# Kernel tuning notes

Hardware: AMD Instinct MI355X
Metric: run time of the kernel (lower is better)

The kernel has to match this reference:

```python
import jax, jax.numpy as jnp
import numpy as np

# Llama-3.2-1B-style int4-quantized decoder (4 layers, reduced vocab)
L, D, H, HD, KVH, DFF, V, B, S = 4, 2048, 32, 64, 8, 8192, 32000, 4, 1024
ROPE_THETA = 500000.0


def setup_inputs() -> dict:
    key = jax.random.key(0)
    ks = jax.random.split(key, 18)
    def qw(k, shape):  # int4 weights stored in int32 carrier, range [-8, 8)
        return jax.random.randint(k, shape, -8, 8, dtype=jnp.int32)
    def sc(k, shape):  # per-output-channel dequant scales
        return jax.random.uniform(k, shape, jnp.float32, 0.005, 0.02)
    DKV = KVH * HD
    return {
        "token_ids": jax.random.randint(ks[0], (B, S), 0, V, dtype=jnp.int32),
        "embed": jax.random.normal(ks[1], (V, D), jnp.float32) * 0.02,
        "gamma_attn": jnp.ones((L, D), jnp.float32),
        "gamma_mlp": jnp.ones((L, D), jnp.float32),
        "gamma_final": jnp.ones((D,), jnp.float32),
        "wq": qw(ks[2], (L, D, D)),   "sq": sc(ks[3], (L, D)),
        "wk": qw(ks[4], (L, DKV, D)), "sk": sc(ks[5], (L, DKV)),
        "wv": qw(ks[6], (L, DKV, D)), "sv": sc(ks[7], (L, DKV)),
        "wo": qw(ks[8], (L, D, D)),   "so": sc(ks[9], (L, D)),
        "wg": qw(ks[10], (L, DFF, D)), "sg": sc(ks[11], (L, DFF)),
        "wu": qw(ks[12], (L, DFF, D)), "su": sc(ks[13], (L, DFF)),
        "wd": qw(ks[14], (L, D, DFF)), "sd": sc(ks[15], (L, D)),
    }


def _rmsnorm(x, g, eps=1e-5):
    return x * jax.lax.rsqrt(jnp.mean(x * x, axis=-1, keepdims=True) + eps) * g


def _rope(x):  # x: [B, S, n_heads, HD], split-half rotation (Llama convention)
    half = HD // 2
    inv_freq = ROPE_THETA ** (-jnp.arange(half, dtype=jnp.float32) * 2.0 / HD)
    ang = jnp.arange(x.shape[1], dtype=jnp.float32)[:, None] * inv_freq  # [S, half]
    cos = jnp.cos(ang)[None, :, None, :]
    sin = jnp.sin(ang)[None, :, None, :]
    x1, x2 = jnp.split(x, 2, axis=-1)
    return jnp.concatenate([x1 * cos - x2 * sin, x1 * sin + x2 * cos], axis=-1)


def _qlin(x, w_int, scale):
    # int4 dequant (per-out-channel symmetric) + matmul: y = x @ (w_int*scale)^T
    w = w_int.astype(jnp.float32) * scale[:, None]
    return jnp.einsum('bsd,od->bso', x, w)


def _forward(token_ids, embed, gamma_attn, gamma_mlp, gamma_final,
             wq, sq, wk, sk, wv, sv, wo, so, wg, sg, wu, su, wd, sd):
    x = embed[token_ids]                                    # [B, S, D]
    causal = jnp.tril(jnp.ones((S, S), dtype=bool))
    for l in range(L):
        # --- attention block ---
        h = _rmsnorm(x, gamma_attn[l])
        q = _qlin(h, wq[l], sq[l]).reshape(B, S, H, HD)
        k = _qlin(h, wk[l], sk[l]).reshape(B, S, KVH, HD)
        v = _qlin(h, wv[l], sv[l]).reshape(B, S, KVH, HD)
        q, k = _rope(q), _rope(k)
        k = jnp.repeat(k, H // KVH, axis=2)                 # GQA expand
        v = jnp.repeat(v, H // KVH, axis=2)
        scores = jnp.einsum('bqhd,bkhd->bhqk', q, k) / np.float32(np.sqrt(HD))
        scores = jnp.where(causal, scores, jnp.float32(-1e9))
        p = jax.nn.softmax(scores, axis=-1)
        attn = jnp.einsum('bhqk,bkhd->bqhd', p, v).reshape(B, S, D)
        x = x + _qlin(attn, wo[l], so[l])
        # --- SwiGLU MLP block ---
        h = _rmsnorm(x, gamma_mlp[l])
        g = jax.nn.silu(_qlin(h, wg[l], sg[l]))
        u = _qlin(h, wu[l], su[l])
        x = x + _qlin(g * u, wd[l], sd[l])
    x = _rmsnorm(x, gamma_final)
    # tied-embedding LM head; next-token logits at last position (decode step)
    return x[:, -1, :] @ embed.T                             # [B, V]


def reference(token_ids, embed, gamma_attn, gamma_mlp, gamma_final,
              wq, sq, wk, sk, wv, sv, wo, so, wg, sg, wu, su, wd, sd):
    return _forward(token_ids, embed, gamma_attn, gamma_mlp, gamma_final,
                    wq, sq, wk, sk, wv, sv, wo, so, wg, sg, wu, su, wd, sd)
```

## Files before the change

kernel.cpp:

```cpp
#include <hip/hip_runtime.h>
#include <hip/hip_bf16.h>

#define D_MODEL 2048
#define NH 32
#define HDIM 64
#define KVHEADS 8
#define DKV 512
#define DFF 8192
#define SEQ 1024
#define BATCH 4
#define NTOK 4096
#define VOCAB 32000
#define NLAYER 4

typedef __attribute__((ext_vector_type(8))) _Float16 f16x8;
typedef __attribute__((ext_vector_type(4))) _Float16 f16x4;
typedef __attribute__((ext_vector_type(4))) float f32x4;
typedef __attribute__((ext_vector_type(4))) int i32x4;

static __device__ __forceinline__ void gload16(const void* g, void* l){
    __builtin_amdgcn_global_load_lds(
        (const __attribute__((address_space(1))) unsigned int*)g,
        (__attribute__((address_space(3))) unsigned int*)l, 16, 0, 0);
}

#define MFMA(d, x, y) d = __builtin_amdgcn_mfma_f32_16x16x32_f16(x, y, d, 0, 0, 0)
#define BAR()    __builtin_amdgcn_s_barrier()
#define LGK0()   do{ asm volatile("s_waitcnt lgkmcnt(0)" ::: "memory"); \
                     __builtin_amdgcn_sched_barrier(0); }while(0)
#define PRIO(x)  __builtin_amdgcn_s_setprio(x)

__global__ __launch_bounds__(256)
void gather_kernel(const int* __restrict__ tok, const float* __restrict__ embed,
                   float* __restrict__ X)
{
    int row = blockIdx.x;
    int id = tok[row];
    const float4* s = (const float4*)(embed + (size_t)id * D_MODEL);
    float4* d = (float4*)(X + (size_t)row * D_MODEL);
    d[threadIdx.x]       = s[threadIdx.x];
    d[threadIdx.x + 256] = s[threadIdx.x + 256];
}

__global__ __launch_bounds__(256)
void rope_table_kernel(float2* __restrict__ rt)
{
    int idx = blockIdx.x * 256 + threadIdx.x;
    int pos = idx >> 5, d = idx & 31;
    float inv = powf(500000.0f, -(float)d * (1.0f / 32.0f));
    float ang = (float)pos * inv;
    float s, c;
    sincosf(ang, &s, &c);
    rt[idx] = make_float2(c, s);
}

__global__ __launch_bounds__(256)
void wconv_all_kernel(const int* __restrict__ wq, const int* __restrict__ wk,
                      const int* __restrict__ wv, const int* __restrict__ wo,
                      const int* __restrict__ wg, const int* __restrict__ wu,
                      const int* __restrict__ wd, _Float16* __restrict__ O)
{
    int i = blockIdx.x * 256 + threadIdx.x;
    const int* s; int loc;
    if      (i <  1048576){ s = wq; loc = i; }
    else if (i <  1310720){ s = wk; loc = i - 1048576; }
    else if (i <  1572864){ s = wv; loc = i - 1310720; }
    else if (i <  2621440){ s = wo; loc = i - 1572864; }
    else if (i <  6815744){ s = wg; loc = i - 2621440; }
    else if (i < 11010048){ s = wu; loc = i - 6815744; }
    else                  { s = wd; loc = i - 11010048; }
    i32x4 w = __builtin_nontemporal_load(&((const i32x4*)s)[loc]);
    f16x4 o;
    o.x = (_Float16)(float)w.x; o.y = (_Float16)(float)w.y;
    o.z = (_Float16)(float)w.z; o.w = (_Float16)(float)w.w;
    __builtin_nontemporal_store(o, &((f16x4*)O)[i]);
}

__global__ __launch_bounds__(256)
void rmsnorm_kernel(const float* __restrict__ X, const float* __restrict__ gamma,
                    _Float16* __restrict__ O)
{
    int row = blockIdx.x;
    const float* x = X + (size_t)row * D_MODEL;
    _Float16* o = O + (size_t)row * D_MODEL;
    int t = threadIdx.x;
    float4 v[2];
    float ss = 0.f;
#pragma unroll
    for (int i = 0; i < 2; i++){
        v[i] = *(const float4*)&x[(t + i*256)*4];
        ss += v[i].x*v[i].x + v[i].y*v[i].y + v[i].z*v[i].z + v[i].w*v[i].w;
    }
    for (int off = 32; off; off >>= 1) ss += __shfl_xor(ss, off, 64);
    __shared__ float red[4];
    __shared__ float invs;
    int lane = t & 63, wid = t >> 6;
    if (lane == 0) red[wid] = ss;
    __syncthreads();
    if (t == 0){
        float s = red[0] + red[1] + red[2] + red[3];
        invs = 1.0f / sqrtf(s / (float)D_MODEL + 1e-5f);
    }
    __syncthreads();
    float inv = invs;
#pragma unroll
    for (int i = 0; i < 2; i++){
        float4 g = *(const float4*)&gamma[(t + i*256)*4];
        f16x4 r;
        r.x = (_Float16)(v[i].x * inv * g.x); r.y = (_Float16)(v[i].y * inv * g.y);
        r.z = (_Float16)(v[i].z * inv * g.z); r.w = (_Float16)(v[i].w * inv * g.w);
        *(f16x4*)&o[(t + i*256)*4] = r;
    }
}

__global__ __launch_bounds__(256)
void final_norm_kernel(const float* __restrict__ X, const float* __restrict__ gamma,
                       float* __restrict__ XF)
{
    int b = blockIdx.x;
    const float* x = X + ((size_t)b * SEQ + SEQ - 1) * D_MODEL;
    float* o = XF + (size_t)b * D_MODEL;
    int t = threadIdx.x;
    float4 v[2];
    float ss = 0.f;
#pragma unroll
    for (int i = 0; i < 2; i++){
        v[i] = *(const float4*)&x[(t + i*256)*4];
        ss += v[i].x*v[i].x + v[i].y*v[i].y + v[i].z*v[i].z + v[i].w*v[i].w;
    }
    for (int off = 32; off; off >>= 1) ss += __shfl_xor(ss, off, 64);
    __shared__ float red[4];
    __shared__ float invs;
    int lane = t & 63, wid = t >> 6;
    if (lane == 0) red[wid] = ss;
    __syncthreads();
    if (t == 0){
        float s = red[0] + red[1] + red[2] + red[3];
        invs = 1.0f / sqrtf(s / (float)D_MODEL + 1e-5f);
    }
    __syncthreads();
    float inv = invs;
#pragma unroll
    for (int i = 0; i < 2; i++){
        float4 g = *(const float4*)&gamma[(t + i*256)*4];
        float4 r;
        r.x = v[i].x * inv * g.x; r.y = v[i].y * inv * g.y;
        r.z = v[i].z * inv * g.z; r.w = v[i].w * inv * g.w;
        *(float4*)&o[(t + i*256)*4] = r;
    }
}

__global__ __launch_bounds__(512, 2)
void gemm_mlp(const _Float16* __restrict__ A, const _Float16* __restrict__ WU,
              const _Float16* __restrict__ WG,
              const float* __restrict__ su, const float* __restrict__ sg,
              _Float16* __restrict__ U, int MT, int NT, int K)
{
    __shared__ __align__(16) _Float16 AS[2][256 * 64];
    __shared__ __align__(16) _Float16 US[2][128 * 64];
    __shared__ __align__(16) _Float16 GS[3][128 * 64];

    int nwg = MT * NT;
    int flat = blockIdx.x;
    int q = nwg >> 3, r = nwg & 7;
    int xcd = flat & 7, lid = flat >> 3;
    int swz = (xcd < r ? xcd * (q + 1) : r * (q + 1) + (xcd - r) * q) + lid;
    int bm = swz % MT, bn = swz / MT;
    int m0 = bm * 256, n0 = bn * 128;

    const int t = threadIdx.x;
    const int lane = t & 63, wid = t >> 6;
    const int ln15 = lane & 15, lq = lane >> 4;
    const int wm = wid >> 1, wn = wid & 1;
    const int sw = ln15 & 7;
    const int sl0 = (lq ^ sw) * 8, sl1 = ((4 + lq) ^ sw) * 8;

    const _Float16* srcA[4]; const _Float16* srcU[2]; const _Float16* srcG[2];
#pragma unroll
    for (int rr = 0; rr < 4; rr++){
        int ch = rr * 512 + t;
        int row = ch >> 3, s = (ch & 7) ^ (row & 7);
        srcA[rr] = A + (size_t)(m0 + row) * K + s * 8;
    }
#pragma unroll
    for (int rr = 0; rr < 2; rr++){
        int ch = rr * 512 + t;
        int row = ch >> 3, s = (ch & 7) ^ (row & 7);
        srcU[rr] = WU + (size_t)(n0 + row) * K + s * 8;
        srcG[rr] = WG + (size_t)(n0 + row) * K + s * 8;
    }
#define STG_A4(tile) do{ int _b = (tile) & 1; \
    gload16(srcA[0] + (size_t)(tile)*64, &AS[_b][(wid*64)*8]); \
    gload16(srcA[1] + (size_t)(tile)*64, &AS[_b][(512 + wid*64)*8]); \
    gload16(srcA[2] + (size_t)(tile)*64, &AS[_b][(1024 + wid*64)*8]); \
    gload16(srcA[3] + (size_t)(tile)*64, &AS[_b][(1536 + wid*64)*8]); }while(0)
#define STG_U2(tile) do{ int _b = (tile) & 1; \
    gload16(srcU[0] + (size_t)(tile)*64, &US[_b][(wid*64)*8]); \
    gload16(srcU[1] + (size_t)(tile)*64, &US[_b][(512 + wid*64)*8]); }while(0)
#define STG_G3(tile) do{ int _b = (tile) % 3; \
    gload16(srcG[0] + (size_t)(tile)*64, &GS[_b][(wid*64)*8]); \
    gload16(srcG[1] + (size_t)(tile)*64, &GS[_b][(512 + wid*64)*8]); }while(0)

    f32x4 accU[4][4], accG[4][4];
#pragma unroll
    for (int i = 0; i < 4; i++)
#pragma unroll
        for (int j = 0; j < 4; j++){
            accU[i][j] = (f32x4){0.f, 0.f, 0.f, 0.f};
            accG[i][j] = (f32x4){0.f, 0.f, 0.f, 0.f};
        }

    const int KT = K >> 6;

    STG_A4(0); STG_U2(0); STG_G3(0); STG_G3(1);
    asm volatile("s_waitcnt vmcnt(2)" ::: "memory");
    BAR();

    for (int kt = 0; kt < KT; ++kt){
        int cur = kt & 1, gcur = kt % 3;
        const _Float16* Ac = AS[cur];
        const _Float16* Uc = US[cur];
        const _Float16* Gc = GS[gcur];
        bool s1 = (kt + 1 < KT), s2 = (kt + 2 < KT);

        f16x8 afk0[4], afk1[4], buk0[4], buk1[4];
#pragma unroll
        for (int mf = 0; mf < 4; mf++)
            afk0[mf] = *(const f16x8*)&Ac[(wm * 64 + mf * 16 + ln15) * 64 + sl0];
#pragma unroll
        for (int nf = 0; nf < 4; nf++)
            buk0[nf] = *(const f16x8*)&Uc[(wn * 64 + nf * 16 + ln15) * 64 + sl0];
        if (s1) STG_A4(kt + 1);
        BAR(); LGK0(); PRIO(1);
#pragma unroll
        for (int mf = 0; mf < 4; mf++)
#pragma unroll
            for (int nf = 0; nf < 4; nf++)
                MFMA(accU[mf][nf], afk0[mf], buk0[nf]);
        PRIO(0); BAR();

#pragma unroll
        for (int mf = 0; mf < 4; mf++)
            afk1[mf] = *(const f16x8*)&Ac[(wm * 64 + mf * 16 + ln15) * 64 + sl1];
#pragma unroll
        for (int nf = 0; nf < 4; nf++)
            buk1[nf] = *(const f16x8*)&Uc[(wn * 64 + nf * 16 + ln15) * 64 + sl1];
        if (s1) STG_U2(kt + 1);
        BAR(); LGK0(); PRIO(1);
#pragma unroll
        for (int mf = 0; mf < 4; mf++)
#pragma unroll
            for (int nf = 0; nf < 4; nf++)
                MFMA(accU[mf][nf], afk1[mf], buk1[nf]);
        PRIO(0); BAR();

        f16x8 bgk0[4], bgk1[4];
#pragma unroll
        for (int nf = 0; nf < 4; nf++){
            bgk0[nf] = *(const f16x8*)&Gc[(wn * 64 + nf * 16 + ln15) * 64 + sl0];
            bgk1[nf] = *(const f16x8*)&Gc[(wn * 64 + nf * 16 + ln15) * 64 + sl1];
        }
        if (s2) STG_G3(kt + 2);
        BAR(); LGK0(); PRIO(1);
#pragma unroll
        for (int mf = 0; mf < 4; mf++)
#pragma unroll
            for (int nf = 0; nf < 4; nf++)
                MFMA(accG[mf][nf], afk0[mf], bgk0[nf]);
        PRIO(0); BAR();

        PRIO(1);
#pragma unroll
        for (int mf = 0; mf < 4; mf++)
#pragma unroll
            for (int nf = 0; nf < 4; nf++)
                MFMA(accG[mf][nf], afk1[mf], bgk1[nf]);
        PRIO(0);
        if (s1){
            if (s2) asm volatile("s_waitcnt vmcnt(2)" ::: "memory");
            else    asm volatile("s_waitcnt vmcnt(0)" ::: "memory");
            BAR();
            __builtin_amdgcn_sched_barrier(0);
        }
    }
#undef STG_A4
#undef STG_U2
#undef STG_G3

#pragma unroll
    for (int mf = 0; mf < 4; mf++){
        int rowb = m0 + wm * 64 + mf * 16 + lq * 4;
#pragma unroll
        for (int nf = 0; nf < 4; nf++){
            int colg = n0 + wn * 64 + nf * 16 + ln15;
            float scu = su[colg], scg = sg[colg];
#pragma unroll
            for (int rr2 = 0; rr2 < 4; rr2++){
                float uv = accU[mf][nf][rr2] * scu;
                float gv = accG[mf][nf][rr2] * scg;
                float sig = 1.0f / (1.0f + expf(-gv));
                U[(size_t)(rowb + rr2) * DFF + colg] = (_Float16)(gv * sig * uv);
            }
        }
    }
}

template<int EPI>
__global__ __launch_bounds__(512, 2)
void gemm_small(const _Float16* __restrict__ A, const _Float16* __restrict__ W,
                const float* __restrict__ sc0, const float* __restrict__ sc1,
                const float* __restrict__ sc2,
                void* __restrict__ C0, void* __restrict__ C1, void* __restrict__ C2,
                const float2* __restrict__ rt,
                int MT, int NT, int N, int K)
{
    __shared__ __align__(16) _Float16 AS[3][128 * 64];
    __shared__ __align__(16) _Float16 BS[3][256 * 64];

    int nwg = MT * NT;
    int flat = blockIdx.x;
    int q = nwg >> 3, r = nwg & 7;
    int xcd = flat & 7, lid = flat >> 3;
    int swz = (xcd < r ? xcd * (q + 1) : r * (q + 1) + (xcd - r) * q) + lid;
    int bm = swz % MT, bn = swz / MT;
    int m0 = bm * 128, n0 = bn * 256;

    const int t = threadIdx.x;
    const int lane = t & 63, wid = t >> 6;
    const int ln15 = lane & 15, lq = lane >> 4;
    const int wm = wid >> 2, wn = wid & 3;
    const int sw = ln15 & 7;
    const int sl0 = (lq ^ sw) * 8, sl1 = ((4 + lq) ^ sw) * 8;

    const _Float16* srcA[2]; const _Float16* srcB[4];
#pragma unroll
    for (int rr = 0; rr < 2; rr++){
        int ch = rr * 512 + t;
        int row = ch >> 3, s = (ch & 7) ^ (row & 7);
        srcA[rr] = A + (size_t)(m0 + row) * K + s * 8;
    }
#pragma unroll
    for (int rr = 0; rr < 4; rr++){
        int ch = rr * 512 + t;
        int row = ch >> 3, s = (ch & 7) ^ (row & 7);
        srcB[rr] = W + (size_t)(n0 + row) * K + s * 8;
    }
#define STG_A3(tile) do{ int _b = (tile) % 3; \
    gload16(srcA[0] + (size_t)(tile)*64, &AS[_b][(wid*64)*8]); \
    gload16(srcA[1] + (size_t)(tile)*64, &AS[_b][(512 + wid*64)*8]); }while(0)
#define STG_B3(tile) do{ int _b = (tile) % 3; \
    gload16(srcB[0] + (size_t)(tile)*64, &BS[_b][(wid*64)*8]); \
    gload16(srcB[1] + (size_t)(tile)*64, &BS[_b][(512 + wid*64)*8]); \
    gload16(srcB[2] + (size_t)(tile)*64, &BS[_b][(1024 + wid*64)*8]); \
    gload16(srcB[3] + (size_t)(tile)*64, &BS[_b][(1536 + wid*64)*8]); }while(0)

    f32x4 acc[4][4];
#pragma unroll
    for (int i = 0; i < 4; i++)
#pragma unroll
        for (int j = 0; j < 4; j++) acc[i][j] = (f32x4){0.f, 0.f, 0.f, 0.f};

    const int KT = K >> 6;

    STG_A3(0); STG_B3(0); STG_A3(1); STG_B3(1);
    asm volatile("s_waitcnt vmcnt(6)" ::: "memory");
    BAR();

    for (int kt = 0; kt < KT; ++kt){
        int cur = kt % 3;
        const _Float16* Ac = AS[cur];
        const _Float16* Bc = BS[cur];
        bool s1 = (kt + 1 < KT), s2 = (kt + 2 < KT);

        f16x8 af0[4], af1[4], bk0[4], bk1[4];
#pragma unroll
        for (int mf = 0; mf < 4; mf++)
            af0[mf] = *(const f16x8*)&Ac[(wm * 64 + mf * 16 + ln15) * 64 + sl0];
#pragma unroll
        for (int nf = 0; nf < 4; nf++)
            bk0[nf] = *(const f16x8*)&Bc[(wn * 64 + nf * 16 + ln15) * 64 + sl0];
        if (s2) STG_B3(kt + 2);
        BAR(); LGK0(); PRIO(1);
#pragma unroll
        for (int mf = 0; mf < 4; mf++)
#pragma unroll
            for (int nf = 0; nf < 4; nf++)
                MFMA(acc[mf][nf], af0[mf], bk0[nf]);
        PRIO(0); BAR();

#pragma unroll
        for (int mf = 0; mf < 4; mf++)
            af1[mf] = *(const f16x8*)&Ac[(wm * 64 + mf * 16 + ln15) * 64 + sl1];
#pragma unroll
        for (int nf = 0; nf < 4; nf++)
            bk1[nf] = *(const f16x8*)&Bc[(wn * 64 + nf * 16 + ln15) * 64 + sl1];
        if (s2) STG_A3(kt + 2);
        BAR(); LGK0(); PRIO(1);
#pragma unroll
        for (int mf = 0; mf < 4; mf++)
#pragma unroll
            for (int nf = 0; nf < 4; nf++)
                MFMA(acc[mf][nf], af1[mf], bk1[nf]);
        PRIO(0);
        if (s1){
            if (s2) asm volatile("s_waitcnt vmcnt(6)" ::: "memory");
            else    asm volatile("s_waitcnt vmcnt(0)" ::: "memory");
            BAR();
            __builtin_amdgcn_sched_barrier(0);
        }
    }
#undef STG_A3
#undef STG_B3

    if (EPI == 3){
        const float* sp; _Float16* dp; int nloc, nstr;
        if (n0 < 2048)      { sp = sc0; dp = (_Float16*)C0; nloc = n0;        nstr = 2048; }
        else if (n0 < 2560) { sp = sc1; dp = (_Float16*)C1; nloc = n0 - 2048; nstr = 512; }
        else                { sp = sc2; dp = (_Float16*)C2; nloc = n0 - 2560; nstr = 512; }
        bool dorope = (n0 < 2560);
        if (dorope){
#pragma unroll
            for (int mf = 0; mf < 4; mf++){
                int rowb = m0 + wm * 64 + mf * 16 + lq * 4;
#pragma unroll
                for (int nf = 0; nf < 2; nf++){
                    int colg = wn * 64 + nf * 16 + ln15;
                    int d = nf * 16 + ln15;
                    float s1v = sp[nloc + colg], s2v = sp[nloc + colg + 32];
#pragma unroll
                    for (int rr2 = 0; rr2 < 4; rr2++){
                        int row = rowb + rr2;
                        int pos = row & (SEQ - 1);
                        float2 cs = rt[pos * 32 + d];
                        float x1 = acc[mf][nf][rr2] * s1v;
                        float x2 = acc[mf][nf + 2][rr2] * s2v;
                        dp[(size_t)row * nstr + nloc + colg]      = (_Float16)(x1 * cs.x - x2 * cs.y);
                        dp[(size_t)row * nstr + nloc + colg + 32] = (_Float16)(x1 * cs.y + x2 * cs.x);
                    }
                }
            }
        } else {
#pragma unroll
            for (int mf = 0; mf < 4; mf++){
                int rowb = m0 + wm * 64 + mf * 16 + lq * 4;
#pragma unroll
                for (int nf = 0; nf < 4; nf++){
                    int colg = wn * 64 + nf * 16 + ln15;
                    float sc = sp[nloc + colg];
#pragma unroll
                    for (int rr2 = 0; rr2 < 4; rr2++)
                        dp[(size_t)(rowb + rr2) * nstr + nloc + colg] =
                            (_Float16)(acc[mf][nf][rr2] * sc);
                }
            }
        }
    } else {
#pragma unroll
        for (int mf = 0; mf < 4; mf++){
            int rowb = m0 + wm * 64 + mf * 16 + lq * 4;
#pragma unroll
            for (int nf = 0; nf < 4; nf++){
                int colg = n0 + wn * 64 + nf * 16 + ln15;
                float sc = sc0[colg];
#pragma unroll
                for (int rr2 = 0; rr2 < 4; rr2++){
                    size_t idx = (size_t)(rowb + rr2) * N + colg;
                    float val = acc[mf][nf][rr2] * sc;
                    if (EPI == 0){
                        ((_Float16*)C0)[idx] = (_Float16)val;
                    } else {
                        ((float*)C0)[idx] += val;
                    }
                }
            }
        }
    }
}

__global__ __launch_bounds__(256)
void attn_kernel(const _Float16* __restrict__ Qb, const _Float16* __restrict__ Kb,
                 const _Float16* __restrict__ Vb, _Float16* __restrict__ Ob)
{
    int bid = blockIdx.x;
    int qt = bid >> 7, h = bid & 31, b = (bid >> 5) & 3;
    int kvh = h >> 2;
    int q0 = qt * 128;
    int t = threadIdx.x, lane = t & 63, wid = t >> 6;
    int ln15 = lane & 15, lq = lane >> 4;

    __shared__ __align__(16) _Float16 Ksm[64 * 72];
    __shared__ __align__(16) _Float16 Vt[64 * 72];
    __shared__ __align__(16) _Float16 Pl[128 * 72];

    f16x8 qf[2][2];
    int qrow_g = b * SEQ + q0 + wid * 32;
#pragma unroll
    for (int mf = 0; mf < 2; mf++)
#pragma unroll
        for (int dc = 0; dc < 2; dc++)
            qf[mf][dc] = *(const f16x8*)(Qb + (size_t)(qrow_g + mf * 16 + ln15) * D_MODEL
                                         + h * HDIM + dc * 32 + lq * 8);

    f32x4 outv[2][4];
#pragma unroll
    for (int i = 0; i < 2; i++)
#pragma unroll
        for (int j = 0; j < 4; j++) outv[i][j] = (f32x4){0.f, 0.f, 0.f, 0.f};
    float mrun[2][4], lrun[2][4];
#pragma unroll
    for (int i = 0; i < 2; i++)
#pragma unroll
        for (int r = 0; r < 4; r++){ mrun[i][r] = -1e30f; lrun[i][r] = 0.f; }

    int ntile = (q0 + 128) >> 6;
    int ld_row = (t + 0) >> 3, ld_c8 = t & 7;
    int ld_row1 = (t + 256) >> 3;

    f16x8 k8[2], v8[2];
    {
        size_t base0 = (size_t)(b * SEQ + ld_row) * DKV + kvh * HDIM + ld_c8 * 8;
        size_t base1 = (size_t)(b * SEQ + ld_row1) * DKV + kvh * HDIM + ld_c8 * 8;
        k8[0] = *(const f16x8*)&Kb[base0];  v8[0] = *(const f16x8*)&Vb[base0];
        k8[1] = *(const f16x8*)&Kb[base1];  v8[1] = *(const f16x8*)&Vb[base1];
    }

    for (int kt = 0; kt < ntile; kt++){
        __syncthreads();
#pragma unroll
        for (int i = 0; i < 2; i++){
            int row = (i == 0) ? ld_row : ld_row1;
            *(f16x8*)&Ksm[row * 72 + ld_c8 * 8] = k8[i];
#pragma unroll
            for (int j = 0; j < 8; j++)
                Vt[(ld_c8 * 8 + j) * 72 + row] = v8[i][j];
        }
        __syncthreads();

        if (kt + 1 < ntile){
            size_t base0 = (size_t)(b * SEQ + (kt + 1) * 64 + ld_row) * DKV + kvh * HDIM + ld_c8 * 8;
            size_t base1 = (size_t)(b * SEQ + (kt + 1) * 64 + ld_row1) * DKV + kvh * HDIM + ld_c8 * 8;
            k8[0] = *(const f16x8*)&Kb[base0];  v8[0] = *(const f16x8*)&Vb[base0];
            k8[1] = *(const f16x8*)&Kb[base1];  v8[1] = *(const f16x8*)&Vb[base1];
        }

#pragma unroll
        for (int mf = 0; mf < 2; mf++){
            f32x4 sa[4];
#pragma unroll
            for (int kvf = 0; kvf < 4; kvf++) sa[kvf] = (f32x4){0.f, 0.f, 0.f, 0.f};
#pragma unroll
            for (int kvf = 0; kvf < 4; kvf++)
#pragma unroll
                for (int dc = 0; dc < 2; dc++){
                    f16x8 kb = *(const f16x8*)&Ksm[(kvf * 16 + ln15) * 72 + dc * 32 + lq * 8];
                    sa[kvf] = __builtin_amdgcn_mfma_f32_16x16x32_f16(qf[mf][dc], kb, sa[kvf], 0, 0, 0);
                }
            int qbase = q0 + wid * 32 + mf * 16 + lq * 4;
            float rowmax[4] = {-1e30f, -1e30f, -1e30f, -1e30f};
#pragma unroll
            for (int kvf = 0; kvf < 4; kvf++){
                int kva = kt * 64 + kvf * 16 + ln15;
#pragma unroll
                for (int r = 0; r < 4; r++){
                    float sv = sa[kvf][r] * 0.125f;
                    if (kva > qbase + r) sv = -1e9f;
                    sa[kvf][r] = sv;
                    rowmax[r] = fmaxf(rowmax[r], sv);
                }
            }
#pragma unroll
            for (int r = 0; r < 4; r++){
                rowmax[r] = fmaxf(rowmax[r], __shfl_xor(rowmax[r], 1, 64));
                rowmax[r] = fmaxf(rowmax[r], __shfl_xor(rowmax[r], 2, 64));
                rowmax[r] = fmaxf(rowmax[r], __shfl_xor(rowmax[r], 4, 64));
                rowmax[r] = fmaxf(rowmax[r], __shfl_xor(rowmax[r], 8, 64));
            }
            float scl[4], rsum[4];
#pragma unroll
            for (int r = 0; r < 4; r++){
                float mo = mrun[mf][r];
                float mn = fmaxf(mo, rowmax[r]);
                scl[r] = expf(mo - mn);
                mrun[mf][r] = mn;
                rsum[r] = 0.f;
            }
#pragma unroll
            for (int kvf = 0; kvf < 4; kvf++)
#pragma unroll
                for (int r = 0; r < 4; r++){
                    float p = expf(sa[kvf][r] - mrun[mf][r]);
                    sa[kvf][r] = p;
                    rsum[r] += p;
                }
#pragma unroll
            for (int r = 0; r < 4; r++){
                rsum[r] += __shfl_xor(rsum[r], 1, 64);
                rsum[r] += __shfl_xor(rsum[r], 2, 64);
                rsum[r] += __shfl_xor(rsum[r], 4, 64);
                rsum[r] += __shfl_xor(rsum[r], 8, 64);
                lrun[mf][r] = lrun[mf][r] * scl[r] + rsum[r];
            }
#pragma unroll
            for (int dfr = 0; dfr < 4; dfr++)
#pragma unroll
                for (int r = 0; r < 4; r++) outv[mf][dfr][r] *= scl[r];
#pragma unroll
            for (int kvf = 0; kvf < 4; kvf++)
#pragma unroll
                for (int r = 0; r < 4; r++)
                    Pl[(wid * 32 + mf * 16 + lq * 4 + r) * 72 + kvf * 16 + ln15] = (_Float16)sa[kvf][r];
        }
        __syncthreads();

#pragma unroll
        for (int mf = 0; mf < 2; mf++)
#pragma unroll
            for (int kc = 0; kc < 2; kc++){
                f16x8 pa = *(const f16x8*)&Pl[(wid * 32 + mf * 16 + ln15) * 72 + kc * 32 + lq * 8];
#pragma unroll
                for (int dfr = 0; dfr < 4; dfr++){
                    f16x8 vb = *(const f16x8*)&Vt[(dfr * 16 + ln15) * 72 + kc * 32 + lq * 8];
                    outv[mf][dfr] = __builtin_amdgcn_mfma_f32_16x16x32_f16(pa, vb, outv[mf][dfr], 0, 0, 0);
                }
            }
    }

#pragma unroll
    for (int mf = 0; mf < 2; mf++)
#pragma unroll
        for (int dfr = 0; dfr < 4; dfr++)
#pragma unroll
            for (int r = 0; r < 4; r++){
                float val = outv[mf][dfr][r] / lrun[mf][r];
                size_t row = (size_t)(b * SEQ + q0 + wid * 32 + mf * 16 + lq * 4 + r);
                Ob[row * D_MODEL + h * HDIM + dfr * 16 + ln15] = (_Float16)val;
            }
}

__global__ __launch_bounds__(256)
void lmhead_kernel(const float* __restrict__ XF, const float* __restrict__ embed,
                   float* __restrict__ out)
{
    __shared__ float xl[4 * D_MODEL];
    int t = threadIdx.x;
#pragma unroll
    for (int i = 0; i < 8; i++){
        int f = t + i * 256;
        ((float4*)xl)[f] = ((const float4*)XF)[f];
    }
    __syncthreads();
    int lane = t & 63, wid = t >> 6;
    for (int rr = 0; rr < 16; rr++){
        int vrow = blockIdx.x * 64 + wid * 16 + rr;
        const float4* er = (const float4*)(embed + (size_t)vrow * D_MODEL);
        float acc[4] = {0.f, 0.f, 0.f, 0.f};
        for (int j = 0; j < 8; j++){
            float4 e = er[lane + 64 * j];
#pragma unroll
            for (int b = 0; b < 4; b++){
                float4 xv = ((float4*)xl)[b * 512 + lane + 64 * j];
                acc[b] += e.x * xv.x + e.y * xv.y + e.z * xv.z + e.w * xv.w;
            }
        }
#pragma unroll
        for (int b = 0; b < 4; b++)
            for (int off = 32; off; off >>= 1) acc[b] += __shfl_xor(acc[b], off, 64);
        if (lane == 0){
#pragma unroll
            for (int b = 0; b < 4; b++)
                out[(size_t)b * VOCAB + vrow] = acc[b];
        }
    }
}

extern "C" void kernel_launch(void* const* d_in, const int* in_sizes, int n_in,
                              void* d_out, int out_size, void* d_ws, size_t ws_size,
                              hipStream_t stream)
{
    const int*   tok   = (const int*)d_in[0];
    const float* embed = (const float*)d_in[1];
    const float* g_attn = (const float*)d_in[2];
    const float* g_mlp  = (const float*)d_in[3];
    const float* g_fin  = (const float*)d_in[4];
    const int*   wq = (const int*)d_in[5];  const float* sq = (const float*)d_in[6];
    const int*   wk = (const int*)d_in[7];  const float* sk = (const float*)d_in[8];
    const int*   wv = (const int*)d_in[9];  const float* sv = (const float*)d_in[10];
    const int*   wo = (const int*)d_in[11]; const float* so = (const float*)d_in[12];
    const int*   wg = (const int*)d_in[13]; const float* sg = (const float*)d_in[14];
    const int*   wu = (const int*)d_in[15]; const float* su = (const float*)d_in[16];
    const int*   wd = (const int*)d_in[17]; const float* sd = (const float*)d_in[18];
    float* out = (float*)d_out;

    char* p = (char*)d_ws;
    _Float16* Wf = (_Float16*)p;  p += (size_t)60817408 * 2;
    float*    X  = (float*)p;     p += (size_t)NTOK * D_MODEL * 4;
    _Float16* Hb = (_Float16*)p;  p += (size_t)NTOK * D_MODEL * 2;
    _Float16* Qb = (_Float16*)p;  p += (size_t)NTOK * D_MODEL * 2;
    _Float16* Kb = (_Float16*)p;  p += (size_t)NTOK * DKV * 2;
    _Float16* Vb = (_Float16*)p;  p += (size_t)NTOK * DKV * 2;
    _Float16* Ab = (_Float16*)p;  p += (size_t)NTOK * D_MODEL * 2;
    _Float16* Ub = (_Float16*)p;  p += (size_t)NTOK * DFF * 2;
    float*    XF = (float*)p;     p += (size_t)BATCH * D_MODEL * 4;
    float2*   RT = (float2*)p;    p += (size_t)SEQ * 32 * 8;

    _Float16* wqf = Wf;
    _Float16* wkf = wqf + (size_t)D_MODEL * D_MODEL;
    _Float16* wvf = wkf + (size_t)DKV * D_MODEL;
    _Float16* wof = wvf + (size_t)DKV * D_MODEL;
    _Float16* wgf = wof + (size_t)D_MODEL * D_MODEL;
    _Float16* wuf = wgf + (size_t)DFF * D_MODEL;
    _Float16* wdf = wuf + (size_t)DFF * D_MODEL;

    gather_kernel<<<NTOK, 256, 0, stream>>>(tok, embed, X);
    rope_table_kernel<<<SEQ * 32 / 256, 256, 0, stream>>>(RT);

    for (int l = 0; l < NLAYER; l++){
        wconv_all_kernel<<<15204352 / 256, 256, 0, stream>>>(
            wq + (size_t)l * D_MODEL * D_MODEL,
            wk + (size_t)l * DKV * D_MODEL,
            wv + (size_t)l * DKV * D_MODEL,
            wo + (size_t)l * D_MODEL * D_MODEL,
            wg + (size_t)l * DFF * D_MODEL,
            wu + (size_t)l * DFF * D_MODEL,
            wd + (size_t)l * D_MODEL * DFF,
            Wf);

        rmsnorm_kernel<<<NTOK, 256, 0, stream>>>(X, g_attn + (size_t)l * D_MODEL, Hb);
        gemm_small<3><<<32 * 12, 512, 0, stream>>>(Hb, wqf,
            sq + (size_t)l * D_MODEL, sk + (size_t)l * DKV, sv + (size_t)l * DKV,
            Qb, Kb, Vb, RT, 32, 12, 3072, D_MODEL);
        attn_kernel<<<1024, 256, 0, stream>>>(Qb, Kb, Vb, Ab);
        gemm_small<1><<<32 * 8, 512, 0, stream>>>(Ab, wof,
            so + (size_t)l * D_MODEL, nullptr, nullptr,
            X, nullptr, nullptr, nullptr, 32, 8, D_MODEL, D_MODEL);

        rmsnorm_kernel<<<NTOK, 256, 0, stream>>>(X, g_mlp + (size_t)l * D_MODEL, Hb);
        gemm_mlp<<<16 * 64, 512, 0, stream>>>(Hb, wuf, wgf,
            su + (size_t)l * DFF, sg + (size_t)l * DFF, Ub, 16, 64, D_MODEL);
        gemm_small<1><<<32 * 8, 512, 0, stream>>>(Ub, wdf,
            sd + (size_t)l * D_MODEL, nullptr, nullptr,
            X, nullptr, nullptr, nullptr, 32, 8, D_MODEL, DFF);
    }

    final_norm_kernel<<<BATCH, 256, 0, stream>>>(X, g_fin, XF);
    lmhead_kernel<<<VOCAB / 64, 256, 0, stream>>>(XF, embed, out);
}
```

Before: 3.211 ms.

## Add split-K 256x256 down-projection GEMM with atomic accumulation into residual

Replaces the gemm_small launch for the MLP down-projection with a new gemm_wd kernel. It reuses the gemm_mlp pipeline structure with a 256x256 output tile, treating the two 128-column halves as the U and G operands. K is split in two across workgroups, which restores the block count to 256 despite the larger tile. Partial results are scaled and added into the residual X with float atomicAdd, trading higher arithmetic intensity for atomic traffic and a non-deterministic summation order.

```diff
diff --git a/kernel.cpp b/kernel.cpp
--- a/kernel.cpp
+++ b/kernel.cpp
@@ -150,6 +150,7 @@
     }
 }
 
+
 __global__ __launch_bounds__(512, 2)
 void gemm_mlp(const _Float16* __restrict__ A, const _Float16* __restrict__ WU,
               const _Float16* __restrict__ WG,
@@ -300,6 +301,164 @@
                 float gv = accG[mf][nf][rr2] * scg;
                 float sig = 1.0f / (1.0f + expf(-gv));
                 U[(size_t)(rowb + rr2) * DFF + colg] = (_Float16)(gv * sig * uv);
+            }
+        }
+    }
+}
+
+__global__ __launch_bounds__(512, 2)
+void gemm_wd(const _Float16* __restrict__ Afull, const _Float16* __restrict__ Wfull,
+             const float* __restrict__ sc, float* __restrict__ C,
+             int MT, int NT, int N, int Kfull)
+{
+    __shared__ __align__(16) _Float16 AS[2][256 * 64];
+    __shared__ __align__(16) _Float16 US[2][128 * 64];
+    __shared__ __align__(16) _Float16 GS[3][128 * 64];
+
+    int flat = blockIdx.x;
+    int kz = flat & 1;
+    int rest = flat >> 1;
+    int nwg = MT * NT;
+    int q = nwg >> 3, r = nwg & 7;
+    int xcd = rest & 7, lid = rest >> 3;
+    int swz = (xcd < r ? xcd * (q + 1) : r * (q + 1) + (xcd - r) * q) + lid;
+    int bm = swz % MT, bn = swz / MT;
+    int m0 = bm * 256, n0 = bn * 256;
+    const int K = Kfull >> 1;
+    const _Float16* A = Afull + (size_t)kz * K;
+    const _Float16* W = Wfull + (size_t)kz * K;
+
+    const int t = threadIdx.x;
+    const int lane = t & 63, wid = t >> 6;
+    const int ln15 = lane & 15, lq = lane >> 4;
+    const int wm = wid >> 1, wn = wid & 1;
+    const int sw = ln15 & 7;
+    const int sl0 = (lq ^ sw) * 8, sl1 = ((4 + lq) ^ sw) * 8;
+
+    const _Float16* srcA[4]; const _Float16* srcU[2]; const _Float16* srcG[2];
+#pragma unroll
+    for (int rr = 0; rr < 4; rr++){
+        int ch = rr * 512 + t;
+        int row = ch >> 3, s = (ch & 7) ^ (row & 7);
+        srcA[rr] = A + (size_t)(m0 + row) * Kfull + s * 8;
+    }
+#pragma unroll
+    for (int rr = 0; rr < 2; rr++){
+        int ch = rr * 512 + t;
+        int row = ch >> 3, s = (ch & 7) ^ (row & 7);
+        srcU[rr] = W + (size_t)(n0 + row) * Kfull + s * 8;
+        srcG[rr] = W + (size_t)(n0 + 128 + row) * Kfull + s * 8;
+    }
+#define STG_A4(tile) do{ int _b = (tile) & 1; \
+    gload16(srcA[0] + (size_t)(tile)*64, &AS[_b][(wid*64)*8]); \
+    gload16(srcA[1] + (size_t)(tile)*64, &AS[_b][(512 + wid*64)*8]); \
+    gload16(srcA[2] + (size_t)(tile)*64, &AS[_b][(1024 + wid*64)*8]); \
+    gload16(srcA[3] + (size_t)(tile)*64, &AS[_b][(1536 + wid*64)*8]); }while(0)
+#define STG_U2(tile) do{ int _b = (tile) & 1; \
+    gload16(srcU[0] + (size_t)(tile)*64, &US[_b][(wid*64)*8]); \
+    gload16(srcU[1] + (size_t)(tile)*64, &US[_b][(512 + wid*64)*8]); }while(0)
+#define STG_G3(tile) do{ int _b = (tile) % 3; \
+    gload16(srcG[0] + (size_t)(tile)*64, &GS[_b][(wid*64)*8]); \
+    gload16(srcG[1] + (size_t)(tile)*64, &GS[_b][(512 + wid*64)*8]); }while(0)
+
+    f32x4 accU[4][4], accG[4][4];
+#pragma unroll
+    for (int i = 0; i < 4; i++)
+#pragma unroll
+        for (int j = 0; j < 4; j++){
+            accU[i][j] = (f32x4){0.f, 0.f, 0.f, 0.f};
+            accG[i][j] = (f32x4){0.f, 0.f, 0.f, 0.f};
+        }
+
+    const int KT = K >> 6;
+
+    STG_A4(0); STG_U2(0); STG_G3(0); STG_G3(1);
+    asm volatile("s_waitcnt vmcnt(2)" ::: "memory");
+    BAR();
+
+    for (int kt = 0; kt < KT; ++kt){
+        int cur = kt & 1, gcur = kt % 3;
+        const _Float16* Ac = AS[cur];
+        const _Float16* Uc = US[cur];
+        const _Float16* Gc = GS[gcur];
+        bool s1 = (kt + 1 < KT), s2 = (kt + 2 < KT);
+
+        f16x8 afk0[4], afk1[4], buk0[4], buk1[4];
+#pragma unroll
+        for (int mf = 0; mf < 4; mf++)
+            afk0[mf] = *(const f16x8*)&Ac[(wm * 64 + mf * 16 + ln15) * 64 + sl0];
+#pragma unroll
+        for (int nf = 0; nf < 4; nf++)
+            buk0[nf] = *(const f16x8*)&Uc[(wn * 64 + nf * 16 + ln15) * 64 + sl0];
+        if (s1) STG_A4(kt + 1);
+        BAR(); LGK0(); PRIO(1);
+#pragma unroll
+        for (int mf = 0; mf < 4; mf++)
+#pragma unroll
+            for (int nf = 0; nf < 4; nf++)
+                MFMA(accU[mf][nf], afk0[mf], buk0[nf]);
+        PRIO(0); BAR();
+
+#pragma unroll
+        for (int mf = 0; mf < 4; mf++)
+            afk1[mf] = *(const f16x8*)&Ac[(wm * 64 + mf * 16 + ln15) * 64 + sl1];
+#pragma unroll
+        for (int nf = 0; nf < 4; nf++)
+            buk1[nf] = *(const f16x8*)&Uc[(wn * 64 + nf * 16 + ln15) * 64 + sl1];
+        if (s1) STG_U2(kt + 1);
+        BAR(); LGK0(); PRIO(1);
+#pragma unroll
+        for (int mf = 0; mf < 4; mf++)
+#pragma unroll
+            for (int nf = 0; nf < 4; nf++)
+                MFMA(accU[mf][nf], afk1[mf], buk1[nf]);
+        PRIO(0); BAR();
+
+        f16x8 bgk0[4], bgk1[4];
+#pragma unroll
+        for (int nf = 0; nf < 4; nf++){
+            bgk0[nf] = *(const f16x8*)&Gc[(wn * 64 + nf * 16 + ln15) * 64 + sl0];
+            bgk1[nf] = *(const f16x8*)&Gc[(wn * 64 + nf * 16 + ln15) * 64 + sl1];
+        }
+        if (s2) STG_G3(kt + 2);
+        BAR(); LGK0(); PRIO(1);
+#pragma unroll
+        for (int mf = 0; mf < 4; mf++)
+#pragma unroll
+            for (int nf = 0; nf < 4; nf++)
+                MFMA(accG[mf][nf], afk0[mf], bgk0[nf]);
+        PRIO(0); BAR();
+
+        PRIO(1);
+#pragma unroll
+        for (int mf = 0; mf < 4; mf++)
+#pragma unroll
+            for (int nf = 0; nf < 4; nf++)
+                MFMA(accG[mf][nf], afk1[mf], bgk1[nf]);
+        PRIO(0);
+        if (s1){
+            if (s2) asm volatile("s_waitcnt vmcnt(2)" ::: "memory");
+            else    asm volatile("s_waitcnt vmcnt(0)" ::: "memory");
+            BAR();
+            __builtin_amdgcn_sched_barrier(0);
+        }
+    }
+#undef STG_A4
+#undef STG_U2
+#undef STG_G3
+
+#pragma unroll
+    for (int mf = 0; mf < 4; mf++){
+        int rowb = m0 + wm * 64 + mf * 16 + lq * 4;
+#pragma unroll
+        for (int nf = 0; nf < 4; nf++){
+            int colU = n0 + wn * 64 + nf * 16 + ln15;
+            int colG = colU + 128;
+            float scu = sc[colU], scg = sc[colG];
+#pragma unroll
+            for (int rr2 = 0; rr2 < 4; rr2++){
+                atomicAdd(&C[(size_t)(rowb + rr2) * N + colU], accU[mf][nf][rr2] * scu);
+                atomicAdd(&C[(size_t)(rowb + rr2) * N + colG], accG[mf][nf][rr2] * scg);
             }
         }
     }
@@ -737,9 +896,8 @@
         rmsnorm_kernel<<<NTOK, 256, 0, stream>>>(X, g_mlp + (size_t)l * D_MODEL, Hb);
         gemm_mlp<<<16 * 64, 512, 0, stream>>>(Hb, wuf, wgf,
             su + (size_t)l * DFF, sg + (size_t)l * DFF, Ub, 16, 64, D_MODEL);
-        gemm_small<1><<<32 * 8, 512, 0, stream>>>(Ub, wdf,
-            sd + (size_t)l * D_MODEL, nullptr, nullptr,
-            X, nullptr, nullptr, nullptr, 32, 8, D_MODEL, DFF);
+        gemm_wd<<<16 * 8 * 2, 512, 0, stream>>>(Ub, wdf,
+            sd + (size_t)l * D_MODEL, X, 16, 8, D_MODEL, DFF);
     }
 
     final_norm_kernel<<<BATCH, 256, 0, stream>>>(X, g_fin, XF);
```

Result: faster. 3.099 ms (-3.5%).
